# Kernel tuning notes

Hardware: AMD Instinct MI355X
Metric: run time of the kernel (lower is better)

## Reference

```python
import jax, jax.numpy as jnp
import numpy as np

N_HEADS = 12

def setup_inputs() -> dict:
    key = jax.random.key(0)
    ks = jax.random.split(key, 3)
    B, C, T = 4, 768, 2048
    x = jax.random.normal(ks[0], (B, C, T), dtype=jnp.float32)
    mask = jnp.ones((B, 1, 1, T), dtype=jnp.int32)  # all valid; masked_fill where mask==0
    Wqkv = jax.random.normal(ks[1], (3 * C, C), dtype=jnp.float32) * 0.02
    bqkv = jnp.zeros((3 * C,), dtype=jnp.float32)
    Wout = jax.random.normal(ks[2], (C, C), dtype=jnp.float32) * 0.02
    bout = jnp.zeros((C,), dtype=jnp.float32)
    return {"x": x, "mask": mask, "Wqkv": Wqkv, "bqkv": bqkv, "Wout": Wout, "bout": bout}


def reference(x, mask, Wqkv, bqkv, Wout, bout):
    B, C, T = x.shape
    H = N_HEADS
    d = C // H
    scale = 1.0 / jnp.sqrt(jnp.asarray(d, x.dtype))
    # 1x1 Conv1d == per-timestep matmul over channels
    qkv = jnp.einsum('oc,bct->bot', Wqkv, x) + bqkv[None, :, None]  # [B,3C,T]
    # channel dim splits as [3, H, d] per the torch view(B,3,H,d,T)
    qkv = qkv.reshape(B, 3, H, d, T).transpose(0, 1, 2, 4, 3)       # [B,3,H,T,d]
    q, k, v = qkv[:, 0], qkv[:, 1], qkv[:, 2]
    score = jnp.einsum('bhtd,bhsd->bhts', q, k) * scale             # [B,H,T,T]
    score = jnp.where(mask == 0, jnp.asarray(-10000.0, score.dtype), score)
    attn = jax.nn.softmax(score, axis=-1)  # dropout: eval mode (identity)
    o = jnp.einsum('bhts,bhsd->bhtd', attn, v)                      # [B,H,T,d]
    o = o.transpose(0, 1, 3, 2).reshape(B, C, T)                    # [B,C,T]
    return jnp.einsum('oc,bct->bot', Wout, o) + bout[None, :, None]
```

## Files before the change

### kernel.cpp

```cpp
#include <hip/hip_runtime.h>
#include <hip/hip_bf16.h>
#include <stdint.h>

#define B_   4
#define C_   768
#define T_   2048
#define H_   12
#define D_   64
#define O3_  2304

typedef __attribute__((ext_vector_type(4))) float f32x4;
typedef __attribute__((ext_vector_type(8))) short bf16x8;

__device__ __forceinline__ unsigned short f2bf(float f) {
  union { float f; unsigned int u; } v; v.f = f;
  unsigned int r = v.u + 0x7fffu + ((v.u >> 16) & 1u);
  return (unsigned short)(r >> 16);
}

__device__ __forceinline__ unsigned int pack2bf(float a, float b) {
  __hip_bfloat162 h2 = __float22bfloat162_rn(make_float2(a, b));
  union { __hip_bfloat162 h; unsigned int u; } cv; cv.h = h2;
  return cv.u;
}

__device__ __forceinline__ float fexp2(float x) {
#if __has_builtin(__builtin_amdgcn_exp2f)
  return __builtin_amdgcn_exp2f(x);
#else
  return exp2f(x);
#endif
}

__device__ __forceinline__ void async16(const void* g, void* lds) {
#if __has_builtin(__builtin_amdgcn_global_load_lds)
  __builtin_amdgcn_global_load_lds((const __attribute__((address_space(1))) void*)g,
                                   (__attribute__((address_space(3))) void*)lds, 16, 0, 0);
#else
  int lane = threadIdx.x & 63;
  *((uint4*)((char*)lds + lane * 16)) = *((const uint4*)g);
#endif
}


__global__ void cvt_f32_bf16(const float* __restrict__ in,
                             unsigned short* __restrict__ out, int n4) {
  int i = blockIdx.x * 256 + threadIdx.x;
  if (i < n4) {
    float4 f = ((const float4*)in)[i];
    ushort4 o;
    o.x = f2bf(f.x); o.y = f2bf(f.y); o.z = f2bf(f.z); o.w = f2bf(f.w);
    ((ushort4*)out)[i] = o;
  }
}

__global__ void make_bias(const int* __restrict__ mask, float* __restrict__ mbias, int n) {
  int i = blockIdx.x * 256 + threadIdx.x;
  if (i < n) mbias[i] = (mask[i] == 0) ? -14426.950408f : 0.0f;
}

__global__ void transpose_x(const float* __restrict__ x,
                            unsigned short* __restrict__ xT) {
  __shared__ unsigned short tile[32][33];
  int b = blockIdx.z;
  int c0 = blockIdx.y * 32;
  int t0 = blockIdx.x * 32;
  int tid = threadIdx.x;
  {
    int cl = tid >> 3;
    int tl = (tid & 7) * 4;
    float4 f = *(const float4*)(x + ((size_t)b * C_ + c0 + cl) * T_ + t0 + tl);
    tile[tl + 0][cl] = f2bf(f.x);
    tile[tl + 1][cl] = f2bf(f.y);
    tile[tl + 2][cl] = f2bf(f.z);
    tile[tl + 3][cl] = f2bf(f.w);
  }
  __syncthreads();
  {
    int tl = tid >> 3;
    int cl = (tid & 7) * 4;
    ushort4 o;
    o.x = tile[tl][cl + 0]; o.y = tile[tl][cl + 1];
    o.z = tile[tl][cl + 2]; o.w = tile[tl][cl + 3];
    *(ushort4*)(xT + ((size_t)b * T_ + t0 + tl) * C_ + c0 + cl) = o;
  }
}

__global__ __launch_bounds__(256)
void gemm_qkv(const unsigned short* __restrict__ xT,
              const unsigned short* __restrict__ W1,
              const float* __restrict__ bqkv,
              unsigned short* __restrict__ Qb,
              unsigned short* __restrict__ Kb,
              unsigned short* __restrict__ Vb) {
  __shared__ unsigned short sA[2][128 * 32];
  __shared__ unsigned short sB[2][128 * 32];

  const int b   = blockIdx.z;
  const int o0  = blockIdx.y * 128;
  const int t0  = blockIdx.x * 128;
  const int tid = threadIdx.x;
  const int wave = tid >> 6, lane = tid & 63;
  const int q = lane >> 4, ln = lane & 15;
  const int tw = wave >> 1, ow = wave & 1;

  const unsigned short* Ax = xT + (size_t)b * T_ * C_;
  const int srow = lane >> 2;
  const int scol = (lane & 3) * 8;

  const f32x4 ZERO = {0.f, 0.f, 0.f, 0.f};
  f32x4 acc[4][4];
#pragma unroll
  for (int mi = 0; mi < 4; ++mi)
#pragma unroll
    for (int ni = 0; ni < 4; ++ni) acc[mi][ni] = ZERO;

#pragma unroll
  for (int j = 0; j < 2; ++j) {
    const int chunk = wave * 2 + j;
    const int row = chunk * 16 + srow;
    async16(Ax + (size_t)(t0 + row) * C_ + scol, &sA[0][chunk * 512]);
    async16(W1 + (size_t)(o0 + row) * C_ + scol, &sB[0][chunk * 512]);
  }

  for (int i = 0; i < 24; ++i) {
    const int buf = i & 1;
    __syncthreads();
    if (i < 23) {
      const int k0 = (i + 1) * 32;
#pragma unroll
      for (int j = 0; j < 2; ++j) {
        const int chunk = wave * 2 + j;
        const int row = chunk * 16 + srow;
        async16(Ax + (size_t)(t0 + row) * C_ + k0 + scol, &sA[buf ^ 1][chunk * 512]);
        async16(W1 + (size_t)(o0 + row) * C_ + k0 + scol, &sB[buf ^ 1][chunk * 512]);
      }
    }

    bf16x8 aF[4], bF[4];
#pragma unroll
    for (int mi = 0; mi < 4; ++mi)
      aF[mi] = *(const bf16x8*)(&sA[buf][(tw * 64 + mi * 16 + ln) * 32 + q * 8]);
#pragma unroll
    for (int ni = 0; ni < 4; ++ni)
      bF[ni] = *(const bf16x8*)(&sB[buf][(ow * 64 + ni * 16 + ln) * 32 + q * 8]);
#pragma unroll
    for (int mi = 0; mi < 4; ++mi)
#pragma unroll
      for (int ni = 0; ni < 4; ++ni)
        acc[mi][ni] = __builtin_amdgcn_mfma_f32_16x16x32_bf16(aF[mi], bF[ni], acc[mi][ni], 0, 0, 0);
  }

  const float QSCL = 0.125f * 1.44269504f;
#pragma unroll
  for (int ni = 0; ni < 4; ++ni) {
    const int o = o0 + ow * 64 + ni * 16 + ln;
    const float bias = bqkv[o];
    const int which = o / C_;
    const int rem = o - which * C_;
    const int bh = b * H_ + (rem >> 6);
    const int dd = rem & 63;
#pragma unroll
    for (int mi = 0; mi < 4; ++mi) {
      const int tb = t0 + tw * 64 + mi * 16 + q * 4;
      f32x4 v = acc[mi][ni];
      if (which == 0) {
#pragma unroll
        for (int r = 0; r < 4; ++r)
          Qb[((size_t)bh * T_ + tb + r) * D_ + dd] = f2bf((v[r] + bias) * QSCL);
      } else if (which == 1) {
#pragma unroll
        for (int r = 0; r < 4; ++r) {
          const int s = tb + r;
          const int cp = (dd >> 3) ^ (s & 7);
          Kb[((size_t)bh * T_ + s) * 64 + (cp << 3) + (dd & 7)] = f2bf(v[r] + bias);
        }
      } else {
        const int tile = tb >> 6, si = tb & 63;
        const int cp = (si >> 3) ^ (dd & 7);
        ushort4 pk;
        pk.x = f2bf(v[0] + bias);
        pk.y = f2bf(v[1] + bias);
        pk.z = f2bf(v[2] + bias);
        pk.w = f2bf(v[3] + bias);
        *(ushort4*)(Vb + (((size_t)bh * 32 + tile) * 64 + dd) * 64 + (cp << 3) + (si & 7)) = pk;
      }
    }
  }
}

__global__ __launch_bounds__(256, 3)
void attn(const unsigned short* __restrict__ Qb,
          const unsigned short* __restrict__ Kb,
          const unsigned short* __restrict__ Vb,
          const float* __restrict__ mbias,
          unsigned short* __restrict__ Ob) {
  __shared__ __align__(16) char smem[32768];
  unsigned short* sK0 = (unsigned short*)smem;
  unsigned short* sV0 = (unsigned short*)(smem + 16384);

  const int id = blockIdx.x;
  const int bh = id % 48;
  const int tblk = id / 48;
  const int b = bh / H_, h = bh % H_;
  const int tid = threadIdx.x, wave = tid >> 6, lane = tid & 63;
  const int q = lane >> 4, ln = lane & 15;
  const int t0w = tblk * 128 + wave * 32;

  bf16x8 Qa[2][2];
#pragma unroll
  for (int tt = 0; tt < 2; ++tt) {
    const unsigned short* qrow = Qb + ((size_t)bh * T_ + t0w + tt * 16 + ln) * D_;
    Qa[tt][0] = *(const bf16x8*)(qrow + q * 8);
    Qa[tt][1] = *(const bf16x8*)(qrow + 32 + q * 8);
  }

  const f32x4 ZERO = {0.f, 0.f, 0.f, 0.f};
  f32x4 Oacc[4][2];
  f32x4 lacc[2];
#pragma unroll
  for (int dt = 0; dt < 4; ++dt)
#pragma unroll
    for (int tt = 0; tt < 2; ++tt) Oacc[dt][tt] = ZERO;
#pragma unroll
  for (int tt = 0; tt < 2; ++tt) lacc[tt] = ZERO;

  const short one_s = (ln == 0) ? (short)0x3F80 : (short)0;
  bf16x8 ones;
#pragma unroll
  for (int j = 0; j < 8; ++j) ones[j] = one_s;

  const unsigned short* gK = Kb + (size_t)bh * T_ * 64;
  const unsigned short* gV = Vb + (size_t)bh * 32 * 4096;
  const float* mb = mbias + b * T_;

  auto stage4 = [&](const unsigned short* g, unsigned short* lds) {
#pragma unroll
    for (int j = 0; j < 2; ++j) {
      const int chunk = wave * 2 + j;
      async16(g + chunk * 512 + lane * 8, lds + chunk * 512);
    }
  };

  auto QK = [&](const unsigned short* sKc, int s0, bf16x8 pfO[2][2]) {
    const float bvl = mb[s0 + lane];
    const bool anymask = (__ballot(bvl != 0.0f) != 0ull);
#pragma unroll
    for (int kc = 0; kc < 2; ++kc) {
      bf16x8 kf0[2], kf1[2];
#pragma unroll
      for (int sb = 0; sb < 2; ++sb) {
        const unsigned short* krow = sKc + (kc * 32 + sb * 16 + ln) * 64;
        kf0[sb] = *(const bf16x8*)(krow + ((q ^ (ln & 7)) << 3));
        kf1[sb] = *(const bf16x8*)(krow + (((4 + q) ^ (ln & 7)) << 3));
      }
#pragma unroll
      for (int tt = 0; tt < 2; ++tt) {
        f32x4 sc[2];
#pragma unroll
        for (int sb = 0; sb < 2; ++sb) {
          f32x4 p0 = __builtin_amdgcn_mfma_f32_16x16x32_bf16(kf0[sb], Qa[tt][0], ZERO, 0, 0, 0);
          sc[sb]   = __builtin_amdgcn_mfma_f32_16x16x32_bf16(kf1[sb], Qa[tt][1], p0, 0, 0, 0);
          if (anymask) {
            f32x4 bb = *(const f32x4*)(mb + s0 + kc * 32 + sb * 16 + q * 4);
#pragma unroll
            for (int r = 0; r < 4; ++r) sc[sb][r] += bb[r];
          }
        }
        unsigned int A0 = pack2bf(fexp2(sc[0][0]), fexp2(sc[0][1]));
        unsigned int B0 = pack2bf(fexp2(sc[0][2]), fexp2(sc[0][3]));
        unsigned int C0 = pack2bf(fexp2(sc[1][0]), fexp2(sc[1][1]));
        unsigned int E0 = pack2bf(fexp2(sc[1][2]), fexp2(sc[1][3]));
        asm volatile("v_permlane32_swap_b32 %0, %1" : "+v"(A0), "+v"(C0));
        asm volatile("v_permlane16_swap_b32 %0, %1" : "+v"(A0), "+v"(C0));
        asm volatile("v_permlane32_swap_b32 %0, %1" : "+v"(B0), "+v"(E0));
        asm volatile("v_permlane16_swap_b32 %0, %1" : "+v"(B0), "+v"(E0));
        union { bf16x8 v; unsigned int u[4]; } P;
        P.u[0] = A0;
        P.u[1] = B0;
        P.u[2] = C0;
        P.u[3] = E0;
        pfO[tt][kc] = P.v;
      }
    }
  };

  auto PV = [&](const unsigned short* sVc, bf16x8 pfI[2][2]) {
#pragma unroll
    for (int dt = 0; dt < 4; ++dt) {
#pragma unroll
      for (int kc = 0; kc < 2; ++kc) {
        bf16x8 vf = *(const bf16x8*)(sVc + (dt * 16 + ln) * 64 +
                                     (((kc * 4 + q) ^ (ln & 7)) << 3));
#pragma unroll
        for (int tt = 0; tt < 2; ++tt)
          Oacc[dt][tt] = __builtin_amdgcn_mfma_f32_16x16x32_bf16(vf, pfI[tt][kc], Oacc[dt][tt], 0, 0, 0);
      }
    }
#pragma unroll
    for (int kc = 0; kc < 2; ++kc)
#pragma unroll
      for (int tt = 0; tt < 2; ++tt)
        lacc[tt] = __builtin_amdgcn_mfma_f32_16x16x32_bf16(ones, pfI[tt][kc], lacc[tt], 0, 0, 0);
  };

  bf16x8 pfA[2][2], pfB[2][2];

  stage4(gK, sK0);
  stage4(gV, sV0);
  __syncthreads();
  stage4(gK + 4096, sK0 + 4096);
  QK(sK0, 0, pfA);

  for (int ith = 0; ith < 15; ++ith) {
    const int it = ith * 2;
    __syncthreads();
    stage4(gK + (size_t)(it + 2) * 4096, sK0);
    stage4(gV + (size_t)(it + 1) * 4096, sV0 + 4096);
    QK(sK0 + 4096, (it + 1) * 64, pfB);
    PV(sV0, pfA);
    __syncthreads();
    stage4(gK + (size_t)(it + 3) * 4096, sK0 + 4096);
    stage4(gV + (size_t)(it + 2) * 4096, sV0);
    QK(sK0, (it + 2) * 64, pfA);
    PV(sV0 + 4096, pfB);
  }

  __syncthreads();
  stage4(gV + (size_t)31 * 4096, sV0 + 4096);
  QK(sK0 + 4096, 31 * 64, pfB);
  PV(sV0, pfA);
  __syncthreads();
  PV(sV0 + 4096, pfB);

#pragma unroll
  for (int tt = 0; tt < 2; ++tt) {
    const float lv = __shfl(lacc[tt][0], ln, 64);
    const float inv = 1.0f / lv;
    const int t = t0w + tt * 16 + ln;
#pragma unroll
    for (int dt = 0; dt < 4; ++dt) {
      f32x4 o = Oacc[dt][tt];
      ushort4 pk;
      pk.x = f2bf(o[0] * inv);
      pk.y = f2bf(o[1] * inv);
      pk.z = f2bf(o[2] * inv);
      pk.w = f2bf(o[3] * inv);
      *(ushort4*)(Ob + ((size_t)b * T_ + t) * C_ + h * D_ + dt * 16 + q * 4) = pk;
    }
  }
}

__global__ __launch_bounds__(256)
void gemm_out(const unsigned short* __restrict__ Ob,
              const unsigned short* __restrict__ W2,
              const float* __restrict__ bout,
              float* __restrict__ out) {
  __shared__ unsigned short sA[2][128 * 32];
  __shared__ unsigned short sB[2][128 * 32];

  const int b   = blockIdx.z;
  const int o0  = blockIdx.y * 128;
  const int t0  = blockIdx.x * 128;
  const int tid = threadIdx.x;
  const int wave = tid >> 6, lane = tid & 63;
  const int q = lane >> 4, ln = lane & 15;
  const int tw = wave >> 1, ow = wave & 1;

  const unsigned short* Bo = Ob + (size_t)b * T_ * C_;
  const int srow = lane >> 2;
  const int scol = (lane & 3) * 8;

  const f32x4 ZERO = {0.f, 0.f, 0.f, 0.f};
  f32x4 acc[4][4];
#pragma unroll
  for (int mi = 0; mi < 4; ++mi)
#pragma unroll
    for (int ni = 0; ni < 4; ++ni) acc[mi][ni] = ZERO;

#pragma unroll
  for (int j = 0; j < 2; ++j) {
    const int chunk = wave * 2 + j;
    const int row = chunk * 16 + srow;
    async16(W2 + (size_t)(o0 + row) * C_ + scol, &sA[0][chunk * 512]);
    async16(Bo + (size_t)(t0 + row) * C_ + scol, &sB[0][chunk * 512]);
  }

  for (int i = 0; i < 24; ++i) {
    const int buf = i & 1;
    __syncthreads();
    if (i < 23) {
      const int k0 = (i + 1) * 32;
#pragma unroll
      for (int j = 0; j < 2; ++j) {
        const int chunk = wave * 2 + j;
        const int row = chunk * 16 + srow;
        async16(W2 + (size_t)(o0 + row) * C_ + k0 + scol, &sA[buf ^ 1][chunk * 512]);
        async16(Bo + (size_t)(t0 + row) * C_ + k0 + scol, &sB[buf ^ 1][chunk * 512]);
      }
    }

    bf16x8 aF[4], bF[4];
#pragma unroll
    for (int mi = 0; mi < 4; ++mi)
      aF[mi] = *(const bf16x8*)(&sA[buf][(tw * 64 + mi * 16 + ln) * 32 + q * 8]);
#pragma unroll
    for (int ni = 0; ni < 4; ++ni)
      bF[ni] = *(const bf16x8*)(&sB[buf][(ow * 64 + ni * 16 + ln) * 32 + q * 8]);
#pragma unroll
    for (int mi = 0; mi < 4; ++mi)
#pragma unroll
      for (int ni = 0; ni < 4; ++ni)
        acc[mi][ni] = __builtin_amdgcn_mfma_f32_16x16x32_bf16(aF[mi], bF[ni], acc[mi][ni], 0, 0, 0);
  }

#pragma unroll
  for (int mi = 0; mi < 4; ++mi) {
    const int ob = o0 + tw * 64 + mi * 16 + q * 4;
#pragma unroll
    for (int ni = 0; ni < 4; ++ni) {
      const int t = t0 + ow * 64 + ni * 16 + ln;
      f32x4 v = acc[mi][ni];
#pragma unroll
      for (int r = 0; r < 4; ++r)
        out[((size_t)b * C_ + ob + r) * T_ + t] = v[r] + bout[ob + r];
    }
  }
}


extern "C" void kernel_launch(void* const* d_in, const int* in_sizes, int n_in,
                              void* d_out, int out_size, void* d_ws, size_t ws_size,
                              hipStream_t stream) {
  (void)in_sizes; (void)n_in; (void)out_size; (void)ws_size;
  const float* x    = (const float*)d_in[0];
  const int*   mask = (const int*)d_in[1];
  const float* Wqkv = (const float*)d_in[2];
  const float* bqkv = (const float*)d_in[3];
  const float* Wout = (const float*)d_in[4];
  const float* bout = (const float*)d_in[5];
  float* out = (float*)d_out;

  const size_t szHead = (size_t)B_ * H_ * T_ * D_;
  const size_t szBTC  = (size_t)B_ * T_ * C_;
  unsigned short* Qb  = (unsigned short*)d_ws;
  unsigned short* Kb  = Qb + szHead;
  unsigned short* Vb  = Kb + szHead;
  unsigned short* Ob  = Vb + szHead;
  unsigned short* xT  = Ob + szBTC;
  unsigned short* W1b = xT + szBTC;
  unsigned short* W2b = W1b + (size_t)O3_ * C_;
  float* mbias        = (float*)(W2b + (size_t)C_ * C_);

  cvt_f32_bf16<<<dim3((O3_ * C_ / 4 + 255) / 256), 256, 0, stream>>>(Wqkv, W1b, O3_ * C_ / 4);
  cvt_f32_bf16<<<dim3((C_ * C_ / 4 + 255) / 256), 256, 0, stream>>>(Wout, W2b, C_ * C_ / 4);
  make_bias<<<dim3((B_ * T_ + 255) / 256), 256, 0, stream>>>(mask, mbias, B_ * T_);
  transpose_x<<<dim3(T_ / 32, C_ / 32, B_), 256, 0, stream>>>(x, xT);
  gemm_qkv<<<dim3(T_ / 128, O3_ / 128, B_), 256, 0, stream>>>(xT, W1b, bqkv, Qb, Kb, Vb);
  attn<<<dim3(768), 256, 0, stream>>>(Qb, Kb, Vb, mbias, Ob);
  gemm_out<<<dim3(T_ / 128, C_ / 128, B_), 256, 0, stream>>>(Ob, W2b, bout, out);
}
```

Baseline: 228.4 us.

## Split attention KV tiles across two wave groups with LDS reduction

The attention block grows from 256 to 512 threads. Two groups of four waves each process one 32-key half of every 64-key tile for the same 128 query rows, and each thread issues one async copy per stage instead of two. At the end, one group writes its partial O and row sums to shared memory and the other group adds them and normalizes. This doubles the waves per block to hide latency and raise occupancy, at the cost of an extra reduction through LDS, more shared memory per block, and redundant Q loads in each group.

Result: slower. 234.8 us (+2.8%).

```diff
diff --git a/kernel.cpp b/kernel.cpp
--- a/kernel.cpp
+++ b/kernel.cpp
@@ -189,13 +189,13 @@
   }
 }
 
-__global__ __launch_bounds__(256, 3)
+__global__ __launch_bounds__(512, 4)
 void attn(const unsigned short* __restrict__ Qb,
           const unsigned short* __restrict__ Kb,
           const unsigned short* __restrict__ Vb,
           const float* __restrict__ mbias,
           unsigned short* __restrict__ Ob) {
-  __shared__ __align__(16) char smem[32768];
+  __shared__ __align__(16) char smem[35328];
   unsigned short* sK0 = (unsigned short*)smem;
   unsigned short* sV0 = (unsigned short*)(smem + 16384);
 
@@ -205,7 +205,8 @@
   const int b = bh / H_, h = bh % H_;
   const int tid = threadIdx.x, wave = tid >> 6, lane = tid & 63;
   const int q = lane >> 4, ln = lane & 15;
-  const int t0w = tblk * 128 + wave * 32;
+  const int wj = wave & 3, si = wave >> 2;
+  const int t0w = tblk * 128 + wj * 32;
 
   bf16x8 Qa[2][2];
 #pragma unroll
@@ -234,119 +235,125 @@
   const unsigned short* gV = Vb + (size_t)bh * 32 * 4096;
   const float* mb = mbias + b * T_;
 
-  auto stage4 = [&](const unsigned short* g, unsigned short* lds) {
-#pragma unroll
-    for (int j = 0; j < 2; ++j) {
-      const int chunk = wave * 2 + j;
-      async16(g + chunk * 512 + lane * 8, lds + chunk * 512);
-    }
+  auto stage1 = [&](const unsigned short* g, unsigned short* lds) {
+    async16(g + wave * 512 + lane * 8, lds + wave * 512);
   };
 
-  auto QK = [&](const unsigned short* sKc, int s0, bf16x8 pfO[2][2]) {
-    const float bvl = mb[s0 + lane];
+  auto QK = [&](const unsigned short* sKc, int s0, bf16x8 pfO[2]) {
+    const float bvl = mb[s0 + si * 32 + (lane & 31)];
     const bool anymask = (__ballot(bvl != 0.0f) != 0ull);
-#pragma unroll
-    for (int kc = 0; kc < 2; ++kc) {
-      bf16x8 kf0[2], kf1[2];
+    bf16x8 kf0[2], kf1[2];
+#pragma unroll
+    for (int sb = 0; sb < 2; ++sb) {
+      const unsigned short* krow = sKc + (si * 32 + sb * 16 + ln) * 64;
+      kf0[sb] = *(const bf16x8*)(krow + ((q ^ (ln & 7)) << 3));
+      kf1[sb] = *(const bf16x8*)(krow + (((4 + q) ^ (ln & 7)) << 3));
+    }
+#pragma unroll
+    for (int tt = 0; tt < 2; ++tt) {
+      f32x4 sc[2];
 #pragma unroll
       for (int sb = 0; sb < 2; ++sb) {
-        const unsigned short* krow = sKc + (kc * 32 + sb * 16 + ln) * 64;
-        kf0[sb] = *(const bf16x8*)(krow + ((q ^ (ln & 7)) << 3));
-        kf1[sb] = *(const bf16x8*)(krow + (((4 + q) ^ (ln & 7)) << 3));
+        f32x4 p0 = __builtin_amdgcn_mfma_f32_16x16x32_bf16(kf0[sb], Qa[tt][0], ZERO, 0, 0, 0);
+        sc[sb]   = __builtin_amdgcn_mfma_f32_16x16x32_bf16(kf1[sb], Qa[tt][1], p0, 0, 0, 0);
+        if (anymask) {
+          f32x4 bb = *(const f32x4*)(mb + s0 + si * 32 + sb * 16 + q * 4);
+#pragma unroll
+          for (int r = 0; r < 4; ++r) sc[sb][r] += bb[r];
+        }
       }
-#pragma unroll
-      for (int tt = 0; tt < 2; ++tt) {
-        f32x4 sc[2];
-#pragma unroll
-        for (int sb = 0; sb < 2; ++sb) {
-          f32x4 p0 = __builtin_amdgcn_mfma_f32_16x16x32_bf16(kf0[sb], Qa[tt][0], ZERO, 0, 0, 0);
-          sc[sb]   = __builtin_amdgcn_mfma_f32_16x16x32_bf16(kf1[sb], Qa[tt][1], p0, 0, 0, 0);
-          if (anymask) {
-            f32x4 bb = *(const f32x4*)(mb + s0 + kc * 32 + sb * 16 + q * 4);
-#pragma unroll
-            for (int r = 0; r < 4; ++r) sc[sb][r] += bb[r];
-          }
-        }
-        unsigned int A0 = pack2bf(fexp2(sc[0][0]), fexp2(sc[0][1]));
-        unsigned int B0 = pack2bf(fexp2(sc[0][2]), fexp2(sc[0][3]));
-        unsigned int C0 = pack2bf(fexp2(sc[1][0]), fexp2(sc[1][1]));
-        unsigned int E0 = pack2bf(fexp2(sc[1][2]), fexp2(sc[1][3]));
-        asm volatile("v_permlane32_swap_b32 %0, %1" : "+v"(A0), "+v"(C0));
-        asm volatile("v_permlane16_swap_b32 %0, %1" : "+v"(A0), "+v"(C0));
-        asm volatile("v_permlane32_swap_b32 %0, %1" : "+v"(B0), "+v"(E0));
-        asm volatile("v_permlane16_swap_b32 %0, %1" : "+v"(B0), "+v"(E0));
-        union { bf16x8 v; unsigned int u[4]; } P;
-        P.u[0] = A0;
-        P.u[1] = B0;
-        P.u[2] = C0;
-        P.u[3] = E0;
-        pfO[tt][kc] = P.v;
-      }
+      unsigned int A0 = pack2bf(fexp2(sc[0][0]), fexp2(sc[0][1]));
+      unsigned int B0 = pack2bf(fexp2(sc[0][2]), fexp2(sc[0][3]));
+      unsigned int C0 = pack2bf(fexp2(sc[1][0]), fexp2(sc[1][1]));
+      unsigned int E0 = pack2bf(fexp2(sc[1][2]), fexp2(sc[1][3]));
+      asm volatile("v_permlane32_swap_b32 %0, %1" : "+v"(A0), "+v"(C0));
+      asm volatile("v_permlane16_swap_b32 %0, %1" : "+v"(A0), "+v"(C0));
+      asm volatile("v_permlane32_swap_b32 %0, %1" : "+v"(B0), "+v"(E0));
+      asm volatile("v_permlane16_swap_b32 %0, %1" : "+v"(B0), "+v"(E0));
+      union { bf16x8 v; unsigned int u[4]; } P;
+      P.u[0] = A0;
+      P.u[1] = B0;
+      P.u[2] = C0;
+      P.u[3] = E0;
+      pfO[tt] = P.v;
     }
   };
 
-  auto PV = [&](const unsigned short* sVc, bf16x8 pfI[2][2]) {
+  auto PV = [&](const unsigned short* sVc, bf16x8 pfI[2]) {
 #pragma unroll
     for (int dt = 0; dt < 4; ++dt) {
-#pragma unroll
-      for (int kc = 0; kc < 2; ++kc) {
-        bf16x8 vf = *(const bf16x8*)(sVc + (dt * 16 + ln) * 64 +
-                                     (((kc * 4 + q) ^ (ln & 7)) << 3));
-#pragma unroll
-        for (int tt = 0; tt < 2; ++tt)
-          Oacc[dt][tt] = __builtin_amdgcn_mfma_f32_16x16x32_bf16(vf, pfI[tt][kc], Oacc[dt][tt], 0, 0, 0);
-      }
-    }
-#pragma unroll
-    for (int kc = 0; kc < 2; ++kc)
+      bf16x8 vf = *(const bf16x8*)(sVc + (dt * 16 + ln) * 64 +
+                                   (((si * 4 + q) ^ (ln & 7)) << 3));
 #pragma unroll
       for (int tt = 0; tt < 2; ++tt)
-        lacc[tt] = __builtin_amdgcn_mfma_f32_16x16x32_bf16(ones, pfI[tt][kc], lacc[tt], 0, 0, 0);
+        Oacc[dt][tt] = __builtin_amdgcn_mfma_f32_16x16x32_bf16(vf, pfI[tt], Oacc[dt][tt], 0, 0, 0);
+    }
+#pragma unroll
+    for (int tt = 0; tt < 2; ++tt)
+      lacc[tt] = __builtin_amdgcn_mfma_f32_16x16x32_bf16(ones, pfI[tt], lacc[tt], 0, 0, 0);
   };
 
-  bf16x8 pfA[2][2], pfB[2][2];
-
-  stage4(gK, sK0);
-  stage4(gV, sV0);
-  __syncthreads();
-  stage4(gK + 4096, sK0 + 4096);
+  bf16x8 pfA[2], pfB[2];
+
+  stage1(gK, sK0);
+  stage1(gV, sV0);
+  __syncthreads();
+  stage1(gK + 4096, sK0 + 4096);
   QK(sK0, 0, pfA);
 
   for (int ith = 0; ith < 15; ++ith) {
     const int it = ith * 2;
     __syncthreads();
-    stage4(gK + (size_t)(it + 2) * 4096, sK0);
-    stage4(gV + (size_t)(it + 1) * 4096, sV0 + 4096);
+    stage1(gK + (size_t)(it + 2) * 4096, sK0);
+    stage1(gV + (size_t)(it + 1) * 4096, sV0 + 4096);
     QK(sK0 + 4096, (it + 1) * 64, pfB);
     PV(sV0, pfA);
     __syncthreads();
-    stage4(gK + (size_t)(it + 3) * 4096, sK0 + 4096);
-    stage4(gV + (size_t)(it + 2) * 4096, sV0);
+    stage1(gK + (size_t)(it + 3) * 4096, sK0 + 4096);
+    stage1(gV + (size_t)(it + 2) * 4096, sV0);
     QK(sK0, (it + 2) * 64, pfA);
     PV(sV0 + 4096, pfB);
   }
 
   __syncthreads();
-  stage4(gV + (size_t)31 * 4096, sV0 + 4096);
+  stage1(gV + (size_t)31 * 4096, sV0 + 4096);
   QK(sK0 + 4096, 31 * 64, pfB);
   PV(sV0, pfA);
   __syncthreads();
   PV(sV0 + 4096, pfB);
 
-#pragma unroll
-  for (int tt = 0; tt < 2; ++tt) {
-    const float lv = __shfl(lacc[tt][0], ln, 64);
-    const float inv = 1.0f / lv;
-    const int t = t0w + tt * 16 + ln;
-#pragma unroll
-    for (int dt = 0; dt < 4; ++dt) {
-      f32x4 o = Oacc[dt][tt];
-      ushort4 pk;
-      pk.x = f2bf(o[0] * inv);
-      pk.y = f2bf(o[1] * inv);
-      pk.z = f2bf(o[2] * inv);
-      pk.w = f2bf(o[3] * inv);
-      *(ushort4*)(Ob + ((size_t)b * T_ + t) * C_ + h * D_ + dt * 16 + q * 4) = pk;
+  __syncthreads();
+  float* fbuf = (float*)smem;
+  float* lbuf = (float*)(smem + 34816);
+  if (si == 1) {
+#pragma unroll
+    for (int tt = 0; tt < 2; ++tt) {
+      const int row = wj * 32 + tt * 16 + ln;
+#pragma unroll
+      for (int dt = 0; dt < 4; ++dt)
+        *(f32x4*)(fbuf + (size_t)row * 68 + dt * 16 + q * 4) = Oacc[dt][tt];
+      if (q == 0) lbuf[row] = lacc[tt][0];
+    }
+  }
+  __syncthreads();
+  if (si == 0) {
+#pragma unroll
+    for (int tt = 0; tt < 2; ++tt) {
+      const int row = wj * 32 + tt * 16 + ln;
+      const float lv = __shfl(lacc[tt][0], ln, 64) + lbuf[row];
+      const float inv = 1.0f / lv;
+      const int t = t0w + tt * 16 + ln;
+#pragma unroll
+      for (int dt = 0; dt < 4; ++dt) {
+        f32x4 p = *(const f32x4*)(fbuf + (size_t)row * 68 + dt * 16 + q * 4);
+        f32x4 o = Oacc[dt][tt];
+        ushort4 pk;
+        pk.x = f2bf((o[0] + p[0]) * inv);
+        pk.y = f2bf((o[1] + p[1]) * inv);
+        pk.z = f2bf((o[2] + p[2]) * inv);
+        pk.w = f2bf((o[3] + p[3]) * inv);
+        *(ushort4*)(Ob + ((size_t)b * T_ + t) * C_ + h * D_ + dt * 16 + q * 4) = pk;
+      }
     }
   }
 }
@@ -457,6 +464,6 @@
   make_bias<<<dim3((B_ * T_ + 255) / 256), 256, 0, stream>>>(mask, mbias, B_ * T_);
   transpose_x<<<dim3(T_ / 32, C_ / 32, B_), 256, 0, stream>>>(x, xT);
   gemm_qkv<<<dim3(T_ / 128, O3_ / 128, B_), 256, 0, stream>>>(xT, W1b, bqkv, Qb, Kb, Vb);
-  attn<<<dim3(768), 256, 0, stream>>>(Qb, Kb, Vb, mbias, Ob);
+  attn<<<dim3(768), 512, 0, stream>>>(Qb, Kb, Vb, mbias, Ob);
   gemm_out<<<dim3(T_ / 128, C_ / 128, B_), 256, 0, stream>>>(Ob, W2b, bout, out);
 }
```

## Triple-buffer K/V tiles in attention with explicit vmcnt waits and precomputed mask bits

Applied to the files above, without the earlier changes.

The attention loop moves from double-buffered K/V shared-memory staging with interleaved QK/PV register ping-pong to a three-stage ring. Two tiles ahead are always in flight, and the plain __syncthreads is replaced by partial s_waitcnt vmcnt(4) barriers. Per-tile mask ballots are precomputed once into a 32-bit mask word. The cost is 48KB of LDS per block instead of 32KB, and QK and PV now run back to back within each step instead of overlapping across tiles.

Result: no change. 227.9 us (-0.2%).

```diff
diff --git a/kernel.cpp b/kernel.cpp
--- a/kernel.cpp
+++ b/kernel.cpp
@@ -195,9 +195,9 @@
           const unsigned short* __restrict__ Vb,
           const float* __restrict__ mbias,
           unsigned short* __restrict__ Ob) {
-  __shared__ __align__(16) char smem[32768];
+  __shared__ __align__(16) char smem[49152];
   unsigned short* sK0 = (unsigned short*)smem;
-  unsigned short* sV0 = (unsigned short*)(smem + 16384);
+  unsigned short* sV0 = (unsigned short*)(smem + 24576);
 
   const int id = blockIdx.x;
   const int bh = id % 48;
@@ -234,7 +234,11 @@
   const unsigned short* gV = Vb + (size_t)bh * 32 * 4096;
   const float* mb = mbias + b * T_;
 
-  auto stage4 = [&](const unsigned short* g, unsigned short* lds) {
+  unsigned int maskbits = 0;
+  for (int t2 = 0; t2 < 32; ++t2)
+    if (__ballot(mb[t2 * 64 + lane] != 0.0f) != 0ull) maskbits |= (1u << t2);
+
+  auto stage = [&](const unsigned short* g, unsigned short* lds) {
 #pragma unroll
     for (int j = 0; j < 2; ++j) {
       const int chunk = wave * 2 + j;
@@ -242,9 +246,22 @@
     }
   };
 
-  auto QK = [&](const unsigned short* sKc, int s0, bf16x8 pfO[2][2]) {
-    const float bvl = mb[s0 + lane];
-    const bool anymask = (__ballot(bvl != 0.0f) != 0ull);
+  auto sync4 = [&]() {
+    __builtin_amdgcn_sched_barrier(0);
+    asm volatile("s_waitcnt vmcnt(4) lgkmcnt(0)" ::: "memory");
+    __builtin_amdgcn_s_barrier();
+    __builtin_amdgcn_sched_barrier(0);
+  };
+  auto sync0 = [&]() {
+    __builtin_amdgcn_sched_barrier(0);
+    asm volatile("s_waitcnt vmcnt(0) lgkmcnt(0)" ::: "memory");
+    __builtin_amdgcn_s_barrier();
+    __builtin_amdgcn_sched_barrier(0);
+  };
+
+  auto QK = [&](const unsigned short* sKc, int it, bf16x8 pfO[2][2]) {
+    const int s0 = it * 64;
+    const bool anymask = (maskbits >> it) & 1;
 #pragma unroll
     for (int kc = 0; kc < 2; ++kc) {
       bf16x8 kf0[2], kf1[2];
@@ -304,34 +321,38 @@
         lacc[tt] = __builtin_amdgcn_mfma_f32_16x16x32_bf16(ones, pfI[tt][kc], lacc[tt], 0, 0, 0);
   };
 
-  bf16x8 pfA[2][2], pfB[2][2];
-
-  stage4(gK, sK0);
-  stage4(gV, sV0);
-  __syncthreads();
-  stage4(gK + 4096, sK0 + 4096);
-  QK(sK0, 0, pfA);
-
-  for (int ith = 0; ith < 15; ++ith) {
-    const int it = ith * 2;
-    __syncthreads();
-    stage4(gK + (size_t)(it + 2) * 4096, sK0);
-    stage4(gV + (size_t)(it + 1) * 4096, sV0 + 4096);
-    QK(sK0 + 4096, (it + 1) * 64, pfB);
-    PV(sV0, pfA);
-    __syncthreads();
-    stage4(gK + (size_t)(it + 3) * 4096, sK0 + 4096);
-    stage4(gV + (size_t)(it + 2) * 4096, sV0);
-    QK(sK0, (it + 2) * 64, pfA);
-    PV(sV0 + 4096, pfB);
-  }
-
-  __syncthreads();
-  stage4(gV + (size_t)31 * 4096, sV0 + 4096);
-  QK(sK0 + 4096, 31 * 64, pfB);
-  PV(sV0, pfA);
-  __syncthreads();
-  PV(sV0 + 4096, pfB);
+  bf16x8 pf[2][2];
+
+  stage(gK, sK0);
+  stage(gV, sV0);
+  stage(gK + 4096, sK0 + 4096);
+  stage(gV + 4096, sV0 + 4096);
+
+  for (int ith = 0; ith < 10; ++ith) {
+    const int it = ith * 3;
+    sync4();
+    stage(gK + (size_t)(it + 2) * 4096, sK0 + 2 * 4096);
+    stage(gV + (size_t)(it + 2) * 4096, sV0 + 2 * 4096);
+    QK(sK0, it, pf);
+    PV(sV0, pf);
+    sync4();
+    stage(gK + (size_t)(it + 3) * 4096, sK0);
+    stage(gV + (size_t)(it + 3) * 4096, sV0);
+    QK(sK0 + 4096, it + 1, pf);
+    PV(sV0 + 4096, pf);
+    sync4();
+    stage(gK + (size_t)(it + 4) * 4096, sK0 + 4096);
+    stage(gV + (size_t)(it + 4) * 4096, sV0 + 4096);
+    QK(sK0 + 2 * 4096, it + 2, pf);
+    PV(sV0 + 2 * 4096, pf);
+  }
+
+  sync4();
+  QK(sK0, 30, pf);
+  PV(sV0, pf);
+  sync0();
+  QK(sK0 + 4096, 31, pf);
+  PV(sV0 + 4096, pf);
 
 #pragma unroll
   for (int tt = 0; tt < 2; ++tt) {
```
